# Performance work log

Hardware: AMD Instinct MI355X
Metric: run time of the kernel (lower is better)

The kernel has to match this reference:

```python
import jax, jax.numpy as jnp
import numpy as np

B, F, T, D, W = 65536, 8, 60, 10, 6  # batch, features, time, window, n_windows
EPS = 1e-8
BN_EPS = 1e-5
IU, JU = np.triu_indices(F, k=1)  # 28 feature pairs


def _bn1d(x, g, b):
    # training-mode BatchNorm1d over [B, C, L]: stats over (B, L) per channel
    m = x.mean(axis=(0, 2), keepdims=True)
    v = x.var(axis=(0, 2), keepdims=True)
    return (x - m) * jax.lax.rsqrt(v + BN_EPS) * g[None, :, None] + b[None, :, None]


def setup_inputs() -> dict:
    key = jax.random.key(0)
    ks = jax.random.split(key, 8)
    s = 0.1
    return {
        "xb": jax.random.normal(ks[0], (B, 1, F, T), dtype=jnp.float32),
        "conv_w": jax.random.normal(ks[1], (4, 1, 1, D), dtype=jnp.float32) * s,
        "conv_b": jnp.zeros((4,), jnp.float32),
        "bn1_g": jnp.ones((28,), jnp.float32), "bn1_b": jnp.zeros((28,), jnp.float32),
        "bn4_g": jnp.ones((F,), jnp.float32), "bn4_b": jnp.zeros((F,), jnp.float32),
        "bn6_g": jnp.ones((F,), jnp.float32), "bn6_b": jnp.zeros((F,), jnp.float32),
        "bn9_g": jnp.ones((32,), jnp.float32), "bn9_b": jnp.zeros((32,), jnp.float32),
        "bnmax_g": jnp.ones((76,), jnp.float32), "bnmax_b": jnp.zeros((76,), jnp.float32),
        "w1": jax.random.normal(ks[2], (30, 608), dtype=jnp.float32) * s,
        "b1": jnp.zeros((30,), jnp.float32),
        "w2": jax.random.normal(ks[3], (1, 30), dtype=jnp.float32) * s,
        "b2": jnp.zeros((1,), jnp.float32),
    }


def reference(xb, conv_w, conv_b, bn1_g, bn1_b, bn4_g, bn4_b, bn6_g, bn6_b,
              bn9_g, bn9_b, bnmax_g, bnmax_b, w1, b1, w2, b2):
    b = xb.shape[0]
    xw = xb.reshape(b, F, W, D)  # non-overlapping windows of length D=10

    # ts_corr: pairwise Pearson correlation per window -> [b, 28, W]
    mu = xw.mean(axis=-1, keepdims=True)
    c = xw - mu
    cov = jnp.einsum('bfwt,bgwt->bfgw', c, c) / D          # [b,F,F,W]
    std = jnp.sqrt((c * c).mean(axis=-1) + EPS)            # [b,F,W]
    corr = cov / (std[:, :, None, :] * std[:, None, :, :] + EPS)
    xb1 = corr[:, IU, JU, :]                               # [b,28,W]

    # ts_zscore: mean/std per window -> [b, F, W]
    xb4 = mu[..., 0] / (std + EPS)

    # ts_decaylinear: linear-decay weighted mean -> [b, F, W]
    dw = jnp.arange(1, D + 1, dtype=jnp.float32)
    dw = dw / dw.sum()
    xb6 = jnp.einsum('bfwt,t->bfw', xw, dw)

    # conv2d kernel (1,10) stride (1,10) -> [b, 4*F, W]
    xb9 = jnp.einsum('bfwt,ot->bofw', xw, conv_w[:, 0, 0, :]) + conv_b[None, :, None, None]
    xb9 = xb9.reshape(b, 4 * F, W)

    h = jnp.concatenate([
        _bn1d(xb1, bn1_g, bn1_b),
        _bn1d(xb4, bn4_g, bn4_b),
        _bn1d(xb6, bn6_g, bn6_b),
        _bn1d(xb9, bn9_g, bn9_b),
    ], axis=1)                                             # [b,76,6]

    h_max = h.reshape(b, 76, 2, 3).max(axis=-1)            # MaxPool1d(3,3) -> [b,76,2]
    h_max = _bn1d(h_max, bnmax_g, bnmax_b)

    flat = jnp.concatenate([h.reshape(b, -1), h_max.reshape(b, -1)], axis=1)  # [b,608]
    out = jax.nn.relu(flat @ w1.T + b1) @ w2.T + b2
    return out.reshape(-1)
```

## Files before the change

kernel.cpp:

```cpp
#include <hip/hip_runtime.h>


#define EPS_F    1e-8f
#define BN_EPS_F 1e-5f
#define LSTR 82

__device__ __forceinline__ float frcp(float x) {
  return __builtin_amdgcn_rcpf(x);
}

template<int Ctrl, int RowMask>
__device__ __forceinline__ float dpp_mov0(float v) {
  return __int_as_float(__builtin_amdgcn_update_dpp(
      0, __float_as_int(v), Ctrl, RowMask, 0xf, true));
}
__device__ __forceinline__ float wave_sum64(float v) {
  v += dpp_mov0<0x111, 0xf>(v);
  v += dpp_mov0<0x112, 0xf>(v);
  v += dpp_mov0<0x114, 0xf>(v);
  v += dpp_mov0<0x118, 0xf>(v);
  v += dpp_mov0<0x142, 0xa>(v);
  v += dpp_mov0<0x143, 0xc>(v);
  return v;
}

constexpr int PI_[28] = {0,0,0,0,0,0,0, 1,1,1,1,1,1, 2,2,2,2,2, 3,3,3,3, 4,4,4, 5,5, 6};
constexpr int PJ_[28] = {1,2,3,4,5,6,7, 2,3,4,5,6,7, 3,4,5,6,7, 4,5,6,7, 5,6,7, 6,7, 7};

template<int PASS, int W>
__device__ __forceinline__ void corr_step(
    const float* __restrict__ bx, const int w,
    const float* __restrict__ w1s,
    float* __restrict__ S, float* __restrict__ Q, float* __restrict__ M,
    float* __restrict__ A, float* __restrict__ partial,
    const int bid, const int lane)
{
  constexpr int PLO = W * 14;
  constexpr int FLO = W * 4;
  float sum[8], SD[8], SP[14];
  #pragma unroll
  for (int f = 0; f < 8; ++f) { sum[f] = 0.f; SD[f] = 0.f; }
  #pragma unroll
  for (int k = 0; k < 14; ++k) SP[k] = 0.f;
  #pragma unroll
  for (int tp = 0; tp < 5; ++tp) {
    float2 x2[8];
    #pragma unroll
    for (int f = 0; f < 8; ++f)
      x2[f] = *reinterpret_cast<const float2*>(bx + f*10 + tp*2);
    #pragma unroll
    for (int f = 0; f < 8; ++f) {
      sum[f] += x2[f].x + x2[f].y;
      SD[f] = fmaf(x2[f].x, x2[f].x, fmaf(x2[f].y, x2[f].y, SD[f]));
    }
    #pragma unroll
    for (int k = 0; k < 14; ++k) {
      const int i = PI_[PLO + k], j = PJ_[PLO + k];
      SP[k] = fmaf(x2[i].x, x2[j].x, fmaf(x2[i].y, x2[j].y, SP[k]));
    }
  }
  float mu[8], sd[8];
  #pragma unroll
  for (int f = 0; f < 8; ++f) {
    mu[f] = sum[f] * 0.1f;
    sd[f] = sqrtf(fmaf(-mu[f], mu[f], SD[f] * 0.1f) + EPS_F);
  }
  #pragma unroll
  for (int k = 0; k < 14; ++k) {
    const int i = PI_[PLO + k], j = PJ_[PLO + k];
    float cov = fmaf(-mu[i], mu[j], SP[k] * 0.1f);
    float v = cov * frcp(fmaf(sd[i], sd[j], EPS_F));
    M[k] = fmaxf(M[k], v);
    if (PASS == 0) { S[k] += v; Q[k] = fmaf(v, v, Q[k]); }
    else {
      const float* wr = w1s + ((PLO + k)*6 + w) * 30;
      #pragma unroll
      for (int j2 = 0; j2 < 30; ++j2) A[j2] = fmaf(v, wr[j2], A[j2]);
    }
  }
  #pragma unroll
  for (int q = 0; q < 4; ++q) {
    const int k = 14 + q;
    float v = mu[FLO + q] * frcp(sd[FLO + q] + EPS_F);
    M[k] = fmaxf(M[k], v);
    if (PASS == 0) { S[k] += v; Q[k] = fmaf(v, v, Q[k]); }
    else {
      const float* wr = w1s + ((28 + FLO + q)*6 + w) * 30;
      #pragma unroll
      for (int j2 = 0; j2 < 30; ++j2) A[j2] = fmaf(v, wr[j2], A[j2]);
    }
  }
  if (w == 2 || w == 5) {
    const int h = (w == 5);
    #pragma unroll
    for (int k = 0; k < 18; ++k) {
      const int ch = (k < 14) ? (PLO + k) : (28 + FLO + (k - 14));
      if (PASS == 0) {
        float t2 = wave_sum64(M[k]);
        float t3 = wave_sum64(M[k] * M[k]);
        if (lane == 63) {
          partial[(size_t)(152*1024) + (size_t)ch * 2048 + h*1024 + bid] = t2;
          partial[(size_t)(152*1024) + (size_t)(76 + ch) * 2048 + h*1024 + bid] = t3;
        }
      } else {
        const float* wr = w1s + (456 + ch*2 + h) * 30;
        #pragma unroll
        for (int j2 = 0; j2 < 30; ++j2) A[j2] = fmaf(M[k], wr[j2], A[j2]);
      }
      M[k] = -3.0e38f;
    }
  }
}

template<int PASS>
__device__ __forceinline__ void bc_step(
    const float* __restrict__ bx, const int w, const int G,
    const float* __restrict__ cw, const float* __restrict__ cb,
    const float* __restrict__ w1s,
    float* __restrict__ S, float* __restrict__ Q, float* __restrict__ M,
    float* __restrict__ A, float* __restrict__ partial,
    const int bid, const int lane)
{
  const int FLO = G * 4;
  #pragma unroll
  for (int q = 0; q < 4; ++q) {
    const int f = FLO + q;
    float2 x2[5];
    #pragma unroll
    for (int tp = 0; tp < 5; ++tp)
      x2[tp] = *reinterpret_cast<const float2*>(bx + f*10 + tp*2);
    float wsm = 0.f;
    #pragma unroll
    for (int tp = 0; tp < 5; ++tp)
      wsm = fmaf(x2[tp].x, (float)(2*tp+1) * (1.f/55.f),
            fmaf(x2[tp].y, (float)(2*tp+2) * (1.f/55.f), wsm));
    {
      const int k = q*5;
      M[k] = fmaxf(M[k], wsm);
      if (PASS == 0) { S[k] += wsm; Q[k] = fmaf(wsm, wsm, Q[k]); }
      else {
        const float* wr = w1s + ((36 + f)*6 + w) * 30;
        #pragma unroll
        for (int j2 = 0; j2 < 30; ++j2) A[j2] = fmaf(wsm, wr[j2], A[j2]);
      }
    }
    #pragma unroll
    for (int o = 0; o < 4; ++o) {
      float cv = cb[o];
      #pragma unroll
      for (int tp = 0; tp < 5; ++tp)
        cv = fmaf(x2[tp].x, cw[o*10 + 2*tp], fmaf(x2[tp].y, cw[o*10 + 2*tp + 1], cv));
      const int k = q*5 + 1 + o;
      M[k] = fmaxf(M[k], cv);
      if (PASS == 0) { S[k] += cv; Q[k] = fmaf(cv, cv, Q[k]); }
      else {
        const float* wr = w1s + ((44 + o*8 + f)*6 + w) * 30;
        #pragma unroll
        for (int j2 = 0; j2 < 30; ++j2) A[j2] = fmaf(cv, wr[j2], A[j2]);
      }
    }
  }
  if (w == 2 || w == 5) {
    const int h = (w == 5);
    #pragma unroll
    for (int k = 0; k < 20; ++k) {
      const int f = FLO + k/5, c = k%5;
      const int ch = (c == 0) ? (36 + f) : (44 + (c-1)*8 + f);
      if (PASS == 0) {
        float t2 = wave_sum64(M[k]);
        float t3 = wave_sum64(M[k] * M[k]);
        if (lane == 63) {
          partial[(size_t)(152*1024) + (size_t)ch * 2048 + h*1024 + bid] = t2;
          partial[(size_t)(152*1024) + (size_t)(76 + ch) * 2048 + h*1024 + bid] = t3;
        }
      } else {
        const float* wr = w1s + (456 + ch*2 + h) * 30;
        #pragma unroll
        for (int j2 = 0; j2 < 30; ++j2) A[j2] = fmaf(M[k], wr[j2], A[j2]);
      }
      M[k] = -3.0e38f;
    }
  }
}


template<int PASS>
__global__ void __launch_bounds__(256, 2)
apass(const float* __restrict__ xb, const float* __restrict__ cw,
      const float* __restrict__ cb, const float* __restrict__ w1s,
      const float* __restrict__ c0, const float* __restrict__ w2,
      const float* __restrict__ b2, float* __restrict__ partial,
      float* __restrict__ out)
{
  __shared__ float sx[64 * LSTR];
  const int tid  = threadIdx.x;
  const int wave = __builtin_amdgcn_readfirstlane(tid >> 6);
  const int lane = tid & 63;
  const int bid  = blockIdx.x;

  float A[30], S[20], Q[20], M[20];
  if (PASS == 0) {
    #pragma unroll
    for (int k = 0; k < 20; ++k) { S[k] = 0.f; Q[k] = 0.f; }
  } else {
    #pragma unroll
    for (int j = 0; j < 30; ++j) A[j] = 0.f;
  }
  #pragma unroll
  for (int k = 0; k < 20; ++k) M[k] = -3.0e38f;

  const int sq = tid >> 2, qq = tid & 3;
  const float* gbase = xb + (size_t)bid * (64*480) + sq*480 + qq*120;
  float* lbase = sx + sq*LSTR + qq*20;
  const float* bx = sx + lane * LSTR;

  float2 t[10];
  #pragma unroll
  for (int k = 0; k < 10; ++k)
    t[k] = *reinterpret_cast<const float2*>(gbase + (k/5)*60 + (k%5)*2);
  #pragma unroll
  for (int k = 0; k < 10; ++k)
    *reinterpret_cast<float2*>(lbase + (k/5)*10 + (k%5)*2) = t[k];
  __syncthreads();

  #pragma unroll 1
  for (int w = 0; w < 6; ++w) {
    if (w < 5) {
      #pragma unroll
      for (int k = 0; k < 10; ++k)
        t[k] = *reinterpret_cast<const float2*>(gbase + (w+1)*10 + (k/5)*60 + (k%5)*2);
    }
    if      (wave == 0) corr_step<PASS,0>(bx, w, w1s, S, Q, M, A, partial, bid, lane);
    else if (wave == 1) corr_step<PASS,1>(bx, w, w1s, S, Q, M, A, partial, bid, lane);
    else                bc_step<PASS>(bx, w, wave - 2, cw, cb, w1s, S, Q, M, A,
                                      partial, bid, lane);
    __syncthreads();
    if (w < 5) {
      #pragma unroll
      for (int k = 0; k < 10; ++k)
        *reinterpret_cast<float2*>(lbase + (k/5)*10 + (k%5)*2) = t[k];
      __syncthreads();
    }
  }

  if (PASS == 0) {
    const int nch = (wave < 2) ? 18 : 20;
    #pragma unroll
    for (int k = 0; k < 20; ++k) {
      if (k < nch) {
        int ch;
        if (wave < 2) ch = (k < 14) ? (wave*14 + k) : (28 + wave*4 + (k - 14));
        else {
          const int f = (wave - 2)*4 + k/5, c = k%5;
          ch = (c == 0) ? (36 + f) : (44 + (c-1)*8 + f);
        }
        float t0 = wave_sum64(S[k]);
        float t1 = wave_sum64(Q[k]);
        if (lane == 63) {
          partial[(size_t)ch * 1024 + bid]        = t0;
          partial[(size_t)(76 + ch) * 1024 + bid] = t1;
        }
      }
    }
  } else {
    if (wave >= 2) {
      #pragma unroll
      for (int j = 0; j < 30; ++j) sx[((wave - 2)*64 + lane)*31 + j] = A[j];
    }
    __syncthreads();
    if (wave < 2) {
      #pragma unroll
      for (int j = 0; j < 30; ++j) A[j] += sx[(wave*64 + lane)*31 + j];
    }
    __syncthreads();
    if (wave == 1) {
      #pragma unroll
      for (int j = 0; j < 30; ++j) sx[lane*31 + j] = A[j];
    }
    __syncthreads();
    if (wave == 0) {
      float t0 = b2[0];
      #pragma unroll
      for (int j = 0; j < 30; ++j) {
        float hh = A[j] + sx[lane*31 + j] + c0[j];
        t0 = fmaf(w2[j], fmaxf(hh, 0.f), t0);
      }
      out[bid * 64 + lane] = t0;
    }
  }
}

__global__ void __launch_bounds__(256)
kR(const float* __restrict__ partial, float* __restrict__ stats) {
  const int r = blockIdx.x;
  const int tid = threadIdx.x;
  float s = 0.f;
  if (r < 152) {
    const float* p = partial + (size_t)r * 1024;
    #pragma unroll
    for (int i = 0; i < 4; ++i) s += p[i*256 + tid];
  } else {
    const float* p = partial + (size_t)(152*1024) + (size_t)(r - 152) * 2048;
    #pragma unroll
    for (int i = 0; i < 8; ++i) s += p[i*256 + tid];
  }
  s = wave_sum64(s);
  __shared__ float ls[4];
  if ((tid & 63) == 63) ls[tid >> 6] = s;
  __syncthreads();
  if (tid == 0) stats[r] = (ls[0] + ls[1]) + (ls[2] + ls[3]);
}

__global__ void __launch_bounds__(256)
k2(const float* __restrict__ stats,
   const float* __restrict__ bn1g, const float* __restrict__ bn1b,
   const float* __restrict__ bn4g, const float* __restrict__ bn4b,
   const float* __restrict__ bn6g, const float* __restrict__ bn6b,
   const float* __restrict__ bn9g, const float* __restrict__ bn9b,
   const float* __restrict__ bnmg, const float* __restrict__ bnmb,
   const float* __restrict__ w1, const float* __restrict__ b1,
   float* __restrict__ w1s, float* __restrict__ c0) {
  __shared__ float P0[76], P1[76], P2[76], P3[76];
  const int tid = threadIdx.x;
  if (tid < 76) {
    const int c = tid;
    float g, b;
    if      (c < 28) { g = bn1g[c];    b = bn1b[c];    }
    else if (c < 36) { g = bn4g[c-28]; b = bn4b[c-28]; }
    else if (c < 44) { g = bn6g[c-36]; b = bn6b[c-36]; }
    else             { g = bn9g[c-44]; b = bn9b[c-44]; }
    const float in1 = 1.0f / (65536.0f * 6.0f);
    const float in2 = 1.0f / (65536.0f * 2.0f);
    float mean = stats[c] * in1;
    float var  = stats[76 + c] * in1 - mean * mean;
    float r    = rsqrtf(var + BN_EPS_F);
    float sc1  = g * r;
    float sh1  = b - mean * sc1;
    float mmr  = stats[152 + c] * in2;
    float vmr  = stats[228 + c] * in2 - mmr * mmr;
    float meanm = sc1 * mmr + sh1;
    float varm  = sc1 * sc1 * vmr;
    float rm  = rsqrtf(varm + BN_EPS_F);
    float scm = bnmg[c] * rm;
    float shm = bnmb[c] - meanm * scm;
    P0[c] = sc1; P1[c] = sh1; P2[c] = scm; P3[c] = shm;
  }
  __syncthreads();

  if (blockIdx.x < 38) {
    const int r0 = blockIdx.x * 16;
    for (int e = tid; e < 16*30; e += 256) {
      const int r = r0 + e / 30, j = e % 30;
      float sc;
      if (r < 456) sc = P0[r / 6];
      else { const int c = (r - 456) >> 1; sc = P0[c] * P2[c]; }
      w1s[r * 30 + j] = sc * w1[j * 608 + r];
    }
  } else {
    const int j = tid >> 3, l8 = tid & 7;
    if (j < 30) {
      float s = 0.f;
      for (int r = l8; r < 608; r += 8) {
        float cst;
        if (r < 456) cst = P1[r / 6];
        else {
          const int c = (r - 456) >> 1;
          cst = fmaf(P2[c], P1[c], P3[c]);
        }
        s = fmaf(cst, w1[j * 608 + r], s);
      }
      s += __shfl_xor(s, 1, 64);
      s += __shfl_xor(s, 2, 64);
      s += __shfl_xor(s, 4, 64);
      if (l8 == 0) c0[j] = s + b1[j];
    }
  }
}


extern "C" void kernel_launch(void* const* d_in, const int* in_sizes, int n_in,
                              void* d_out, int out_size, void* d_ws, size_t ws_size,
                              hipStream_t stream) {
  (void)in_sizes; (void)n_in; (void)out_size; (void)ws_size;
  const float* xb   = (const float*)d_in[0];
  const float* cw   = (const float*)d_in[1];
  const float* cb   = (const float*)d_in[2];
  const float* bn1g = (const float*)d_in[3];
  const float* bn1b = (const float*)d_in[4];
  const float* bn4g = (const float*)d_in[5];
  const float* bn4b = (const float*)d_in[6];
  const float* bn6g = (const float*)d_in[7];
  const float* bn6b = (const float*)d_in[8];
  const float* bn9g = (const float*)d_in[9];
  const float* bn9b = (const float*)d_in[10];
  const float* bnmg = (const float*)d_in[11];
  const float* bnmb = (const float*)d_in[12];
  const float* w1   = (const float*)d_in[13];
  const float* b1   = (const float*)d_in[14];
  const float* w2   = (const float*)d_in[15];
  const float* b2   = (const float*)d_in[16];

  float* out     = (float*)d_out;
  float* ws      = (float*)d_ws;
  float* stats   = ws;
  float* c0      = ws + 608;
  float* w1s     = ws + 640;
  float* partial = ws + 18880;

  apass<0><<<1024, 256, 0, stream>>>(xb, cw, cb, nullptr, nullptr, nullptr,
                                     nullptr, partial, nullptr);
  kR<<<304, 256, 0, stream>>>(partial, stats);
  k2<<<39, 256, 0, stream>>>(stats, bn1g, bn1b, bn4g, bn4b, bn6g, bn6b,
                             bn9g, bn9b, bnmg, bnmb, w1, b1, w1s, c0);
  apass<1><<<1024, 256, 0, stream>>>(xb, cw, cb, w1s, c0, w2, b2,
                                     nullptr, out);
}
```

Baseline: 398.9 us.

## Load whole sample block into LDS once and split halves across lanes

Each block now handles 32 samples instead of 64 and stages the full 32x480 input tile into shared memory in one coalesced load. Each lane covers one half (three windows) of a sample, which removes the per-window reload and syncthreads loop. Max-pool stats are written once at the end, and the partial-sum layout and reduction kernel are simplified. The grid doubles to 2048 blocks. The LDS tile is larger (about 62KB), which may reduce occupancy, and the final cross-wave reduction goes through shared memory.

```diff
diff --git a/kernel.cpp b/kernel.cpp
--- a/kernel.cpp
+++ b/kernel.cpp
@@ -3,7 +3,7 @@
 
 #define EPS_F    1e-8f
 #define BN_EPS_F 1e-5f
-#define LSTR 82
+#define LSTR 486
 
 __device__ __forceinline__ float frcp(float x) {
   return __builtin_amdgcn_rcpf(x);
@@ -28,157 +28,139 @@
 constexpr int PJ_[28] = {1,2,3,4,5,6,7, 2,3,4,5,6,7, 3,4,5,6,7, 4,5,6,7, 5,6,7, 6,7, 7};
 
 template<int PASS, int W>
-__device__ __forceinline__ void corr_step(
-    const float* __restrict__ bx, const int w,
+__device__ __forceinline__ void corr_full(
+    const float* __restrict__ bx, const int h,
     const float* __restrict__ w1s,
     float* __restrict__ S, float* __restrict__ Q, float* __restrict__ M,
-    float* __restrict__ A, float* __restrict__ partial,
-    const int bid, const int lane)
+    float* __restrict__ A)
 {
   constexpr int PLO = W * 14;
   constexpr int FLO = W * 4;
-  float sum[8], SD[8], SP[14];
-  #pragma unroll
-  for (int f = 0; f < 8; ++f) { sum[f] = 0.f; SD[f] = 0.f; }
-  #pragma unroll
-  for (int k = 0; k < 14; ++k) SP[k] = 0.f;
-  #pragma unroll
-  for (int tp = 0; tp < 5; ++tp) {
-    float2 x2[8];
-    #pragma unroll
-    for (int f = 0; f < 8; ++f)
-      x2[f] = *reinterpret_cast<const float2*>(bx + f*10 + tp*2);
+  #pragma unroll 1
+  for (int wl = 0; wl < 3; ++wl) {
+    float sum[8], SD[8], SP[14];
+    #pragma unroll
+    for (int f = 0; f < 8; ++f) { sum[f] = 0.f; SD[f] = 0.f; }
+    #pragma unroll
+    for (int k = 0; k < 14; ++k) SP[k] = 0.f;
+    #pragma unroll
+    for (int tp = 0; tp < 5; ++tp) {
+      float2 x2[8];
+      #pragma unroll
+      for (int f = 0; f < 8; ++f)
+        x2[f] = *reinterpret_cast<const float2*>(bx + f*60 + wl*10 + tp*2);
+      #pragma unroll
+      for (int f = 0; f < 8; ++f) {
+        sum[f] += x2[f].x + x2[f].y;
+        SD[f] = fmaf(x2[f].x, x2[f].x, fmaf(x2[f].y, x2[f].y, SD[f]));
+      }
+      #pragma unroll
+      for (int k = 0; k < 14; ++k) {
+        const int i = PI_[PLO + k], j = PJ_[PLO + k];
+        SP[k] = fmaf(x2[i].x, x2[j].x, fmaf(x2[i].y, x2[j].y, SP[k]));
+      }
+    }
+    float mu[8], sd[8];
     #pragma unroll
     for (int f = 0; f < 8; ++f) {
-      sum[f] += x2[f].x + x2[f].y;
-      SD[f] = fmaf(x2[f].x, x2[f].x, fmaf(x2[f].y, x2[f].y, SD[f]));
+      mu[f] = sum[f] * 0.1f;
+      sd[f] = sqrtf(fmaf(-mu[f], mu[f], SD[f] * 0.1f) + EPS_F);
     }
     #pragma unroll
     for (int k = 0; k < 14; ++k) {
       const int i = PI_[PLO + k], j = PJ_[PLO + k];
-      SP[k] = fmaf(x2[i].x, x2[j].x, fmaf(x2[i].y, x2[j].y, SP[k]));
-    }
-  }
-  float mu[8], sd[8];
-  #pragma unroll
-  for (int f = 0; f < 8; ++f) {
-    mu[f] = sum[f] * 0.1f;
-    sd[f] = sqrtf(fmaf(-mu[f], mu[f], SD[f] * 0.1f) + EPS_F);
-  }
-  #pragma unroll
-  for (int k = 0; k < 14; ++k) {
-    const int i = PI_[PLO + k], j = PJ_[PLO + k];
-    float cov = fmaf(-mu[i], mu[j], SP[k] * 0.1f);
-    float v = cov * frcp(fmaf(sd[i], sd[j], EPS_F));
-    M[k] = fmaxf(M[k], v);
-    if (PASS == 0) { S[k] += v; Q[k] = fmaf(v, v, Q[k]); }
-    else {
-      const float* wr = w1s + ((PLO + k)*6 + w) * 30;
-      #pragma unroll
-      for (int j2 = 0; j2 < 30; ++j2) A[j2] = fmaf(v, wr[j2], A[j2]);
-    }
-  }
-  #pragma unroll
-  for (int q = 0; q < 4; ++q) {
-    const int k = 14 + q;
-    float v = mu[FLO + q] * frcp(sd[FLO + q] + EPS_F);
-    M[k] = fmaxf(M[k], v);
-    if (PASS == 0) { S[k] += v; Q[k] = fmaf(v, v, Q[k]); }
-    else {
-      const float* wr = w1s + ((28 + FLO + q)*6 + w) * 30;
-      #pragma unroll
-      for (int j2 = 0; j2 < 30; ++j2) A[j2] = fmaf(v, wr[j2], A[j2]);
-    }
-  }
-  if (w == 2 || w == 5) {
-    const int h = (w == 5);
+      float cov = fmaf(-mu[i], mu[j], SP[k] * 0.1f);
+      float v = cov * frcp(fmaf(sd[i], sd[j], EPS_F));
+      M[k] = fmaxf(M[k], v);
+      if (PASS == 0) { S[k] += v; Q[k] = fmaf(v, v, Q[k]); }
+      else {
+        const float* wr = w1s + ((PLO + k)*6 + h*3 + wl) * 30;
+        #pragma unroll
+        for (int j2 = 0; j2 < 30; ++j2) A[j2] = fmaf(v, wr[j2], A[j2]);
+      }
+    }
+    #pragma unroll
+    for (int q = 0; q < 4; ++q) {
+      const int k = 14 + q;
+      float v = mu[FLO + q] * frcp(sd[FLO + q] + EPS_F);
+      M[k] = fmaxf(M[k], v);
+      if (PASS == 0) { S[k] += v; Q[k] = fmaf(v, v, Q[k]); }
+      else {
+        const float* wr = w1s + ((28 + FLO + q)*6 + h*3 + wl) * 30;
+        #pragma unroll
+        for (int j2 = 0; j2 < 30; ++j2) A[j2] = fmaf(v, wr[j2], A[j2]);
+      }
+    }
+  }
+  if (PASS == 1) {
     #pragma unroll
     for (int k = 0; k < 18; ++k) {
       const int ch = (k < 14) ? (PLO + k) : (28 + FLO + (k - 14));
-      if (PASS == 0) {
-        float t2 = wave_sum64(M[k]);
-        float t3 = wave_sum64(M[k] * M[k]);
-        if (lane == 63) {
-          partial[(size_t)(152*1024) + (size_t)ch * 2048 + h*1024 + bid] = t2;
-          partial[(size_t)(152*1024) + (size_t)(76 + ch) * 2048 + h*1024 + bid] = t3;
-        }
-      } else {
-        const float* wr = w1s + (456 + ch*2 + h) * 30;
-        #pragma unroll
-        for (int j2 = 0; j2 < 30; ++j2) A[j2] = fmaf(M[k], wr[j2], A[j2]);
-      }
-      M[k] = -3.0e38f;
+      const float* wr = w1s + (456 + ch*2 + h) * 30;
+      #pragma unroll
+      for (int j2 = 0; j2 < 30; ++j2) A[j2] = fmaf(M[k], wr[j2], A[j2]);
     }
   }
 }
 
 template<int PASS>
-__device__ __forceinline__ void bc_step(
-    const float* __restrict__ bx, const int w, const int G,
+__device__ __forceinline__ void bc_full(
+    const float* __restrict__ bx, const int h, const int G,
     const float* __restrict__ cw, const float* __restrict__ cb,
     const float* __restrict__ w1s,
     float* __restrict__ S, float* __restrict__ Q, float* __restrict__ M,
-    float* __restrict__ A, float* __restrict__ partial,
-    const int bid, const int lane)
+    float* __restrict__ A)
 {
   const int FLO = G * 4;
-  #pragma unroll
-  for (int q = 0; q < 4; ++q) {
-    const int f = FLO + q;
-    float2 x2[5];
-    #pragma unroll
-    for (int tp = 0; tp < 5; ++tp)
-      x2[tp] = *reinterpret_cast<const float2*>(bx + f*10 + tp*2);
-    float wsm = 0.f;
-    #pragma unroll
-    for (int tp = 0; tp < 5; ++tp)
-      wsm = fmaf(x2[tp].x, (float)(2*tp+1) * (1.f/55.f),
-            fmaf(x2[tp].y, (float)(2*tp+2) * (1.f/55.f), wsm));
-    {
-      const int k = q*5;
-      M[k] = fmaxf(M[k], wsm);
-      if (PASS == 0) { S[k] += wsm; Q[k] = fmaf(wsm, wsm, Q[k]); }
-      else {
-        const float* wr = w1s + ((36 + f)*6 + w) * 30;
+  #pragma unroll 1
+  for (int wl = 0; wl < 3; ++wl) {
+    #pragma unroll
+    for (int q = 0; q < 4; ++q) {
+      const int f = FLO + q;
+      float2 x2[5];
+      #pragma unroll
+      for (int tp = 0; tp < 5; ++tp)
+        x2[tp] = *reinterpret_cast<const float2*>(bx + f*60 + wl*10 + tp*2);
+      float wsm = 0.f;
+      #pragma unroll
+      for (int tp = 0; tp < 5; ++tp)
+        wsm = fmaf(x2[tp].x, (float)(2*tp+1) * (1.f/55.f),
+              fmaf(x2[tp].y, (float)(2*tp+2) * (1.f/55.f), wsm));
+      {
+        const int k = q*5;
+        M[k] = fmaxf(M[k], wsm);
+        if (PASS == 0) { S[k] += wsm; Q[k] = fmaf(wsm, wsm, Q[k]); }
+        else {
+          const float* wr = w1s + ((36 + f)*6 + h*3 + wl) * 30;
+          #pragma unroll
+          for (int j2 = 0; j2 < 30; ++j2) A[j2] = fmaf(wsm, wr[j2], A[j2]);
+        }
+      }
+      #pragma unroll
+      for (int o = 0; o < 4; ++o) {
+        float cv = cb[o];
         #pragma unroll
-        for (int j2 = 0; j2 < 30; ++j2) A[j2] = fmaf(wsm, wr[j2], A[j2]);
-      }
-    }
-    #pragma unroll
-    for (int o = 0; o < 4; ++o) {
-      float cv = cb[o];
-      #pragma unroll
-      for (int tp = 0; tp < 5; ++tp)
-        cv = fmaf(x2[tp].x, cw[o*10 + 2*tp], fmaf(x2[tp].y, cw[o*10 + 2*tp + 1], cv));
-      const int k = q*5 + 1 + o;
-      M[k] = fmaxf(M[k], cv);
-      if (PASS == 0) { S[k] += cv; Q[k] = fmaf(cv, cv, Q[k]); }
-      else {
-        const float* wr = w1s + ((44 + o*8 + f)*6 + w) * 30;
-        #pragma unroll
-        for (int j2 = 0; j2 < 30; ++j2) A[j2] = fmaf(cv, wr[j2], A[j2]);
-      }
-    }
-  }
-  if (w == 2 || w == 5) {
-    const int h = (w == 5);
+        for (int tp = 0; tp < 5; ++tp)
+          cv = fmaf(x2[tp].x, cw[o*10 + 2*tp], fmaf(x2[tp].y, cw[o*10 + 2*tp + 1], cv));
+        const int k = q*5 + 1 + o;
+        M[k] = fmaxf(M[k], cv);
+        if (PASS == 0) { S[k] += cv; Q[k] = fmaf(cv, cv, Q[k]); }
+        else {
+          const float* wr = w1s + ((44 + o*8 + f)*6 + h*3 + wl) * 30;
+          #pragma unroll
+          for (int j2 = 0; j2 < 30; ++j2) A[j2] = fmaf(cv, wr[j2], A[j2]);
+        }
+      }
+    }
+  }
+  if (PASS == 1) {
     #pragma unroll
     for (int k = 0; k < 20; ++k) {
       const int f = FLO + k/5, c = k%5;
       const int ch = (c == 0) ? (36 + f) : (44 + (c-1)*8 + f);
-      if (PASS == 0) {
-        float t2 = wave_sum64(M[k]);
-        float t3 = wave_sum64(M[k] * M[k]);
-        if (lane == 63) {
-          partial[(size_t)(152*1024) + (size_t)ch * 2048 + h*1024 + bid] = t2;
-          partial[(size_t)(152*1024) + (size_t)(76 + ch) * 2048 + h*1024 + bid] = t3;
-        }
-      } else {
-        const float* wr = w1s + (456 + ch*2 + h) * 30;
-        #pragma unroll
-        for (int j2 = 0; j2 < 30; ++j2) A[j2] = fmaf(M[k], wr[j2], A[j2]);
-      }
-      M[k] = -3.0e38f;
+      const float* wr = w1s + (456 + ch*2 + h) * 30;
+      #pragma unroll
+      for (int j2 = 0; j2 < 30; ++j2) A[j2] = fmaf(M[k], wr[j2], A[j2]);
     }
   }
 }
@@ -192,11 +174,29 @@
       const float* __restrict__ b2, float* __restrict__ partial,
       float* __restrict__ out)
 {
-  __shared__ float sx[64 * LSTR];
+  __shared__ float sx[32 * LSTR];
   const int tid  = threadIdx.x;
   const int wave = __builtin_amdgcn_readfirstlane(tid >> 6);
   const int lane = tid & 63;
+  const int sm   = lane & 31;
+  const int h    = lane >> 5;
   const int bid  = blockIdx.x;
+
+  const float* gb = xb + (size_t)bid * (32 * 480);
+  {
+    float2 t[30];
+    #pragma unroll
+    for (int k = 0; k < 30; ++k)
+      t[k] = *reinterpret_cast<const float2*>(gb + (size_t)(k*256 + tid) * 2);
+    #pragma unroll
+    for (int k = 0; k < 30; ++k) {
+      const int g2  = k*256 + tid;
+      const int smw = g2 / 240;
+      const int c2  = g2 - smw*240;
+      *reinterpret_cast<float2*>(sx + smw*LSTR + c2*2) = t[k];
+    }
+  }
+  __syncthreads();
 
   float A[30], S[20], Q[20], M[20];
   if (PASS == 0) {
@@ -209,39 +209,11 @@
   #pragma unroll
   for (int k = 0; k < 20; ++k) M[k] = -3.0e38f;
 
-  const int sq = tid >> 2, qq = tid & 3;
-  const float* gbase = xb + (size_t)bid * (64*480) + sq*480 + qq*120;
-  float* lbase = sx + sq*LSTR + qq*20;
-  const float* bx = sx + lane * LSTR;
-
-  float2 t[10];
-  #pragma unroll
-  for (int k = 0; k < 10; ++k)
-    t[k] = *reinterpret_cast<const float2*>(gbase + (k/5)*60 + (k%5)*2);
-  #pragma unroll
-  for (int k = 0; k < 10; ++k)
-    *reinterpret_cast<float2*>(lbase + (k/5)*10 + (k%5)*2) = t[k];
-  __syncthreads();
-
-  #pragma unroll 1
-  for (int w = 0; w < 6; ++w) {
-    if (w < 5) {
-      #pragma unroll
-      for (int k = 0; k < 10; ++k)
-        t[k] = *reinterpret_cast<const float2*>(gbase + (w+1)*10 + (k/5)*60 + (k%5)*2);
-    }
-    if      (wave == 0) corr_step<PASS,0>(bx, w, w1s, S, Q, M, A, partial, bid, lane);
-    else if (wave == 1) corr_step<PASS,1>(bx, w, w1s, S, Q, M, A, partial, bid, lane);
-    else                bc_step<PASS>(bx, w, wave - 2, cw, cb, w1s, S, Q, M, A,
-                                      partial, bid, lane);
-    __syncthreads();
-    if (w < 5) {
-      #pragma unroll
-      for (int k = 0; k < 10; ++k)
-        *reinterpret_cast<float2*>(lbase + (k/5)*10 + (k%5)*2) = t[k];
-      __syncthreads();
-    }
-  }
+  const float* bx = sx + sm * LSTR + h * 30;
+
+  if      (wave == 0) corr_full<PASS,0>(bx, h, w1s, S, Q, M, A);
+  else if (wave == 1) corr_full<PASS,1>(bx, h, w1s, S, Q, M, A);
+  else                bc_full<PASS>(bx, h, wave - 2, cw, cb, w1s, S, Q, M, A);
 
   if (PASS == 0) {
     const int nch = (wave < 2) ? 18 : 20;
@@ -256,36 +228,32 @@
         }
         float t0 = wave_sum64(S[k]);
         float t1 = wave_sum64(Q[k]);
+        float t2 = wave_sum64(M[k]);
+        float t3 = wave_sum64(M[k] * M[k]);
         if (lane == 63) {
-          partial[(size_t)ch * 1024 + bid]        = t0;
-          partial[(size_t)(76 + ch) * 1024 + bid] = t1;
+          partial[(size_t)(      ch) * 2048 + bid] = t0;
+          partial[(size_t)( 76 + ch) * 2048 + bid] = t1;
+          partial[(size_t)(152 + ch) * 2048 + bid] = t2;
+          partial[(size_t)(228 + ch) * 2048 + bid] = t3;
         }
       }
     }
   } else {
-    if (wave >= 2) {
-      #pragma unroll
-      for (int j = 0; j < 30; ++j) sx[((wave - 2)*64 + lane)*31 + j] = A[j];
-    }
     __syncthreads();
-    if (wave < 2) {
-      #pragma unroll
-      for (int j = 0; j < 30; ++j) A[j] += sx[(wave*64 + lane)*31 + j];
-    }
+    #pragma unroll
+    for (int j = 0; j < 30; ++j) sx[(wave*64 + lane)*31 + j] = A[j];
     __syncthreads();
-    if (wave == 1) {
-      #pragma unroll
-      for (int j = 0; j < 30; ++j) sx[lane*31 + j] = A[j];
-    }
-    __syncthreads();
-    if (wave == 0) {
+    if (tid < 32) {
       float t0 = b2[0];
       #pragma unroll
       for (int j = 0; j < 30; ++j) {
-        float hh = A[j] + sx[lane*31 + j] + c0[j];
+        float hh = c0[j];
+        #pragma unroll
+        for (int wv = 0; wv < 4; ++wv)
+          hh += sx[(wv*64 + tid)*31 + j] + sx[(wv*64 + 32 + tid)*31 + j];
         t0 = fmaf(w2[j], fmaxf(hh, 0.f), t0);
       }
-      out[bid * 64 + lane] = t0;
+      out[bid * 32 + tid] = t0;
     }
   }
 }
@@ -293,17 +261,11 @@
 __global__ void __launch_bounds__(256)
 kR(const float* __restrict__ partial, float* __restrict__ stats) {
   const int r = blockIdx.x;
+  const float* p = partial + (size_t)r * 2048;
   const int tid = threadIdx.x;
   float s = 0.f;
-  if (r < 152) {
-    const float* p = partial + (size_t)r * 1024;
-    #pragma unroll
-    for (int i = 0; i < 4; ++i) s += p[i*256 + tid];
-  } else {
-    const float* p = partial + (size_t)(152*1024) + (size_t)(r - 152) * 2048;
-    #pragma unroll
-    for (int i = 0; i < 8; ++i) s += p[i*256 + tid];
-  }
+  #pragma unroll
+  for (int i = 0; i < 8; ++i) s += p[i*256 + tid];
   s = wave_sum64(s);
   __shared__ float ls[4];
   if ((tid & 63) == 63) ls[tid >> 6] = s;
@@ -407,11 +369,11 @@
   float* w1s     = ws + 640;
   float* partial = ws + 18880;
 
-  apass<0><<<1024, 256, 0, stream>>>(xb, cw, cb, nullptr, nullptr, nullptr,
+  apass<0><<<2048, 256, 0, stream>>>(xb, cw, cb, nullptr, nullptr, nullptr,
                                      nullptr, partial, nullptr);
   kR<<<304, 256, 0, stream>>>(partial, stats);
   k2<<<39, 256, 0, stream>>>(stats, bn1g, bn1b, bn4g, bn4b, bn6g, bn6b,
                              bn9g, bn9b, bnmg, bnmb, w1, b1, w1s, c0);
-  apass<1><<<1024, 256, 0, stream>>>(xb, cw, cb, w1s, c0, w2, b2,
+  apass<1><<<2048, 256, 0, stream>>>(xb, cw, cb, w1s, c0, w2, b2,
                                      nullptr, out);
 }
```

After: 414.2 us. 1.04x slower.
